# Optimization experiments

Hardware: AMD Instinct MI355X
Metric: run time of the kernel (lower is better)

Reference implementation:

```python
import jax, jax.numpy as jnp
import numpy as np

NUM_USERS = 100000
NUM_ITEMS = 50000
EMBED_DIM = 64
N_LAYERS = 3
NNZ = 4800000
BATCH = 16384
N_NODES = NUM_USERS + NUM_ITEMS


def setup_inputs() -> dict:
    key = jax.random.key(0)
    k1, k2, k3, k4, k5, k6, k7 = jax.random.split(key, 7)
    users = jax.random.randint(k1, (BATCH,), 0, NUM_USERS, dtype=jnp.int64 if jax.config.jax_enable_x64 else jnp.int32)
    items = jax.random.randint(k2, (BATCH,), 0, NUM_ITEMS, dtype=jnp.int64 if jax.config.jax_enable_x64 else jnp.int32)
    adj_rows = jax.random.randint(k3, (NNZ,), 0, N_NODES, dtype=jnp.int32)
    adj_cols = jax.random.randint(k4, (NNZ,), 0, N_NODES, dtype=jnp.int32)
    adj_vals = jax.random.uniform(k5, (NNZ,), dtype=jnp.float32)
    user_emb = jax.random.normal(k6, (NUM_USERS, EMBED_DIM), dtype=jnp.float32)
    item_emb = jax.random.normal(k7, (NUM_ITEMS, EMBED_DIM), dtype=jnp.float32)
    return {"users": users, "items": items, "adj_rows": adj_rows,
            "adj_cols": adj_cols, "adj_vals": adj_vals,
            "user_emb": user_emb, "item_emb": item_emb}


def _spmm(rows, cols, vals, x):
    # y = A @ x for COO sparse A: gather source rows, scale, scatter-add to dest
    return jax.ops.segment_sum(vals[:, None] * x[cols], rows, num_segments=N_NODES)


def reference(users, items, adj_rows, adj_cols, adj_vals, user_emb, item_emb):
    ego = jnp.concatenate([user_emb, item_emb], axis=0)  # [N_NODES, D]
    acc = ego
    cur = ego
    for _ in range(N_LAYERS):
        cur = _spmm(adj_rows, adj_cols, adj_vals, cur)
        acc = acc + cur
    mean_emb = acc / jnp.float32(N_LAYERS + 1)
    user_final = mean_emb[:NUM_USERS]
    item_final = mean_emb[NUM_USERS:]
    u = user_final[users]  # [B, D]
    i = item_final[items]  # [B, D]
    return jnp.sum(u * i, axis=-1)  # [B]
```

## Files before the change

### kernel.cpp

```cpp
#include <hip/hip_runtime.h>
#include <hip/hip_bf16.h>

#define NUM_USERS 100000
#define NUM_ITEMS 50000
#define EMBED_DIM 64
#define N_NODES   150000
#define ROW_SHIFT 9
#define ROWS_PER_BUCKET 512
#define B_BUCKETS ((N_NODES + ROWS_PER_BUCKET - 1) / ROWS_PER_BUCKET)
#define NBP 512
#define BIN_CHUNK 2048
#define PLACE_CHUNK 2048
#define COL_MASK 0x3FFFF

typedef unsigned short ushort_t;
typedef unsigned int uint_t;

__device__ __forceinline__ float bf16_to_f32(ushort_t u) {
    return __uint_as_float(((unsigned)u) << 16);
}
__device__ __forceinline__ ushort_t f32_to_bf16(float f) {
    return __builtin_bit_cast(ushort_t, __float2bfloat16(f));
}

__device__ __forceinline__ void scan512(int c, int t, int* wsum,
                                        int* excl_out, int* total_out) {
    int lane = t & 63, wv = t >> 6;
    int x = c;
#pragma unroll
    for (int d = 1; d < 64; d <<= 1) {
        int y = __shfl_up(x, d, 64);
        if (lane >= d) x += y;
    }
    if (lane == 63) wsum[wv] = x;
    __syncthreads();
    if (t < 64) {
        int s = (lane < 8) ? wsum[lane] : 0;
#pragma unroll
        for (int d = 1; d < 8; d <<= 1) {
            int y = __shfl_up(s, d, 64);
            if (lane >= d) s += y;
        }
        if (lane < 8) wsum[lane] = s;
    }
    __syncthreads();
    int off = (wv > 0) ? wsum[wv - 1] : 0;
    *excl_out = x + off - c;
    *total_out = wsum[7];
}

__global__ void __launch_bounds__(512) k_bin2(const float* __restrict__ ue,
                                              const float* __restrict__ ie,
                                              ushort_t* __restrict__ xb,
                                              const int* __restrict__ rows,
                                              const int* __restrict__ cols,
                                              const float* __restrict__ vals,
                                              int* __restrict__ cursor,
                                              int2* __restrict__ staging,
                                              int nnz, int cap, int g_conv) {
    int t = threadIdx.x;
    if ((int)blockIdx.x < g_conv) {
        int i = blockIdx.x * 512 + t;
        const int n4 = (N_NODES * EMBED_DIM) / 4;
        if (i >= n4) return;
        const int usplit = (NUM_USERS * EMBED_DIM) / 4;
        float4 f = (i < usplit) ? ((const float4*)ue)[i] : ((const float4*)ie)[i - usplit];
        ushort4 o;
        o.x = f32_to_bf16(f.x);
        o.y = f32_to_bf16(f.y);
        o.z = f32_to_bf16(f.z);
        o.w = f32_to_bf16(f.w);
        ((ushort4*)xb)[i] = o;
        return;
    }

    __shared__ int  ccnt[NBP];
    __shared__ int  cpos[NBP];
    __shared__ int  gdst[NBP];
    __shared__ int  wsum[8];
    __shared__ int2 entries[BIN_CHUNK];
    __shared__ ushort_t ebuck[BIN_CHUNK];

    int base = (blockIdx.x - g_conv) * BIN_CHUNK;
    ccnt[t] = 0;
    __syncthreads();

    int   myrow[BIN_CHUNK / 512];
    int   mycol[BIN_CHUNK / 512];
    float myval[BIN_CHUNK / 512];
#pragma unroll
    for (int k = 0; k < BIN_CHUNK / 512; k++) {
        int idx = base + k * 512 + t;
        int r = (idx < nnz) ? rows[idx] : -1;
        myrow[k] = r;
        if (r >= 0) {
            mycol[k] = cols[idx];
            myval[k] = vals[idx];
            atomicAdd(&ccnt[r >> ROW_SHIFT], 1);
        }
    }
    __syncthreads();

    int c = ccnt[t];
    int excl, total;
    scan512(c, t, wsum, &excl, &total);
    cpos[t] = excl;
    __syncthreads();

#pragma unroll
    for (int k = 0; k < BIN_CHUNK / 512; k++) {
        int r = myrow[k];
        if (r >= 0) {
            int b = r >> ROW_SHIFT;
            int lrow = r & (ROWS_PER_BUCKET - 1);
            int slot = atomicAdd(&cpos[b], 1);
            entries[slot] = make_int2(mycol[k] | (lrow << 18), __float_as_int(myval[k]));
            ebuck[slot] = (ushort_t)b;
        }
    }
    __syncthreads();

    if (t < B_BUCKETS && ccnt[t] > 0) {
        int g = atomicAdd(&cursor[t], ccnt[t]);
        gdst[t] = t * cap + g - (cpos[t] - ccnt[t]);
    }
    __syncthreads();

    for (int i = t; i < total; i += 512) {
        int eb = ebuck[i];
        int pos = gdst[eb] + i;
        if (pos < (eb + 1) * cap)
            staging[pos] = entries[i];
    }
}

__global__ void __launch_bounds__(512) k_hist(const int2* __restrict__ staging,
                                              const int* __restrict__ cursor,
                                              int* __restrict__ H,
                                              int cap, int chunks) {
    __shared__ int h[ROWS_PER_BUCKET];
    int b = blockIdx.x / chunks;
    int k = blockIdx.x - b * chunks;
    int t = threadIdx.x;
    h[t] = 0;
    __syncthreads();
    int cnt_b = cursor[b];
    if (cnt_b > cap) cnt_b = cap;
    int hi = k * PLACE_CHUNK + PLACE_CHUNK;
    if (hi > cnt_b) hi = cnt_b;
    int rbase = b * cap;
#pragma unroll 1
    for (int i = k * PLACE_CHUNK + t; i < hi; i += 512)
        atomicAdd(&h[staging[rbase + i].x >> 18], 1);
    __syncthreads();
    H[(size_t)blockIdx.x * ROWS_PER_BUCKET + t] = h[t];
}

__global__ void __launch_bounds__(512) k_scan2(int* __restrict__ H,
                                               int2* __restrict__ ranges,
                                               int cap, int chunks) {
    __shared__ int wsum[8];
    int b = blockIdx.x;
    int t = threadIdx.x;
    size_t base = (size_t)b * chunks * ROWS_PER_BUCKET + t;
    int c = 0;
#pragma unroll 1
    for (int k = 0; k < chunks; k++) c += H[base + (size_t)k * ROWS_PER_BUCKET];
    int excl, total;
    scan512(c, t, wsum, &excl, &total);
    (void)total;
    int row = (b << ROW_SHIFT) + t;
    int beg = b * cap + excl;
    if (row < N_NODES) ranges[row] = make_int2(beg, beg + c);
    int s = beg;
#pragma unroll 1
    for (int k = 0; k < chunks; k++) {
        int hh = H[base + (size_t)k * ROWS_PER_BUCKET];
        H[base + (size_t)k * ROWS_PER_BUCKET] = s;
        s += hh;
    }
}

__global__ void __launch_bounds__(512) k_place2(const int2* __restrict__ staging,
                                                const int* __restrict__ cursor,
                                                const int* __restrict__ H,
                                                int2* __restrict__ cv,
                                                int cap, int chunks) {
    __shared__ int c[ROWS_PER_BUCKET];
    int b = blockIdx.x / chunks;
    int k = blockIdx.x - b * chunks;
    int t = threadIdx.x;
    c[t] = H[(size_t)blockIdx.x * ROWS_PER_BUCKET + t];
    __syncthreads();
    int cnt_b = cursor[b];
    if (cnt_b > cap) cnt_b = cap;
    int hi = k * PLACE_CHUNK + PLACE_CHUNK;
    if (hi > cnt_b) hi = cnt_b;
    int rbase = b * cap;
#pragma unroll 1
    for (int i = k * PLACE_CHUNK + t; i < hi; i += 512) {
        int2 e = staging[rbase + i];
        int pos = atomicAdd(&c[e.x >> 18], 1);
        cv[pos] = make_int2(e.x & COL_MASK, e.y);
    }
}

#define ISSUE8(R, J0)                                                         \
    _Pragma("unroll")                                                         \
    for (int j = 0; j < 8; j++) {                                             \
        int sc = __builtin_amdgcn_readlane(vc, (J0) + j);                     \
        R[j] = xb[((size_t)(uint_t)sc << 6) + lane];                          \
    }

#define CONS8(R, J0)                                                          \
    _Pragma("unroll")                                                         \
    for (int j = 0; j < 8; j++) {                                             \
        float sv = __uint_as_float((uint_t)__builtin_amdgcn_readlane(vv, (J0) + j)); \
        acc += sv * __uint_as_float((uint_t)R[j] << 16);                      \
    }

__device__ __forceinline__ float spmm_row_rl(int beg, int end, int lane,
                                             const int2* __restrict__ cv,
                                             const ushort_t* __restrict__ xb) {
    float acc = 0.f;
#pragma unroll 1
    for (int b = beg; b < end; b += 64) {
        int2 ed = cv[b + lane];
        bool lv = (b + lane) < end;
        int vc = lv ? ed.x : 0;
        int vv = lv ? ed.y : 0;
        int rem = end - b;
        if (rem > 64) rem = 64;

        ushort_t q0[8], q1[8], q2[8], q3[8];
        ISSUE8(q0, 0)
        if (rem > 8)  { ISSUE8(q1, 8)  }
        if (rem > 16) { ISSUE8(q2, 16) }
        if (rem > 24) { ISSUE8(q3, 24) }
        CONS8(q0, 0)
        if (rem > 8)  { CONS8(q1, 8)  }
        if (rem > 16) { CONS8(q2, 16) }
        if (rem > 24) { CONS8(q3, 24) }
        if (rem > 32) {
            ISSUE8(q0, 32)
            if (rem > 40) { ISSUE8(q1, 40) }
            if (rem > 48) { ISSUE8(q2, 48) }
            if (rem > 56) { ISSUE8(q3, 56) }
            CONS8(q0, 32)
            if (rem > 40) { CONS8(q1, 40) }
            if (rem > 48) { CONS8(q2, 48) }
            if (rem > 56) { CONS8(q3, 56) }
        }
    }
    return acc;
}

__global__ void k_spmm(const int2* __restrict__ ranges, const int2* __restrict__ cv,
                       const ushort_t* __restrict__ xb, ushort_t* __restrict__ out) {
    int row = (blockIdx.x * blockDim.x + threadIdx.x) >> 6;
    int lane = threadIdx.x & 63;
    if (row >= N_NODES) return;
    row = __builtin_amdgcn_readfirstlane(row);
    int2 rng = ranges[row];
    int beg = __builtin_amdgcn_readfirstlane(rng.x);
    int end = __builtin_amdgcn_readfirstlane(rng.y);
    float a = spmm_row_rl(beg, end, lane, cv, xb);
    out[(size_t)row * 64 + lane] = f32_to_bf16(a);
}

__global__ void k_last(const int2* __restrict__ ranges, const int2* __restrict__ cv,
                       const int* __restrict__ users, const int* __restrict__ items,
                       const float* __restrict__ ue, const float* __restrict__ ie,
                       const ushort_t* __restrict__ xbA, const ushort_t* __restrict__ xbB,
                       float* __restrict__ out, int batch) {
    __shared__ float uv[2][64];
    int lane  = threadIdx.x & 63;
    int lwave = threadIdx.x >> 6;
    int gwave = (int)blockIdx.x * 4 + lwave;
    int w     = gwave >> 1;
    int side  = gwave & 1;
    bool valid = w < batch;

    int beg = 0, end = 0, row = 0, idxv = 0;
    if (valid) {
        idxv = __builtin_amdgcn_readfirstlane(side ? items[w] : users[w]);
        row  = side ? NUM_USERS + idxv : idxv;
        int2 rng = ranges[row];
        beg = __builtin_amdgcn_readfirstlane(rng.x);
        end = __builtin_amdgcn_readfirstlane(rng.y);
    }
    float a = spmm_row_rl(beg, end, lane, cv, xbB);

    float x_ = 0.f;
    if (valid) {
        float e = side ? ie[(size_t)idxv * EMBED_DIM + lane]
                       : ue[(size_t)idxv * EMBED_DIM + lane];
        float A = bf16_to_f32(xbA[(size_t)row * 64 + lane]);
        float B = bf16_to_f32(xbB[(size_t)row * 64 + lane]);
        x_ = e + A + B + a;
    }
    int slot = lwave >> 1;
    if (valid && side == 0) uv[slot][lane] = x_;
    __syncthreads();
    if (valid && side == 1) {
        float p = x_ * uv[slot][lane];
#pragma unroll
        for (int d = 32; d > 0; d >>= 1) p += __shfl_down(p, d, 64);
        if (lane == 0) out[w] = p * (1.0f / 16.0f);
    }
}


extern "C" void kernel_launch(void* const* d_in, const int* in_sizes, int n_in,
                              void* d_out, int out_size, void* d_ws, size_t ws_size,
                              hipStream_t stream) {
    const int*   users    = (const int*)  d_in[0];
    const int*   items    = (const int*)  d_in[1];
    const int*   adj_rows = (const int*)  d_in[2];
    const int*   adj_cols = (const int*)  d_in[3];
    const float* adj_vals = (const float*)d_in[4];
    const float* user_emb = (const float*)d_in[5];
    const float* item_emb = (const float*)d_in[6];
    float* out = (float*)d_out;

    const int batch = in_sizes[0];
    const int nnz   = in_sizes[2];

    int cap = ((nnz / B_BUCKETS) * 9 + 7) / 8;
    cap = (cap + 63) & ~63;
    const size_t padded = (size_t)B_BUCKETS * cap;
    const int chunks = (cap + PLACE_CHUNK - 1) / PLACE_CHUNK;

    char* p = (char*)d_ws;
    auto alloc = [&](size_t bytes) -> char* {
        char* r = p;
        p += (bytes + 255) & ~(size_t)255;
        return r;
    };
    const size_t xb_bytes = (size_t)N_NODES * EMBED_DIM * 2;
    int2*     ranges = (int2*) alloc((size_t)N_NODES * 8);
    int*      cursor = (int*)  alloc(NBP * 4);
    int*      H      = (int*)  alloc((size_t)B_BUCKETS * chunks * ROWS_PER_BUCKET * 4);
    int2*     cv     = (int2*) alloc(padded * 8);
    size_t    region_bytes = padded * 8;
    if (region_bytes < 2 * xb_bytes) region_bytes = 2 * xb_bytes;
    char*     region  = alloc(region_bytes);
    int2*     staging = (int2*)region;
    ushort_t* xbA     = (ushort_t*)region;
    ushort_t* xbB     = (ushort_t*)(region + xb_bytes);
    ushort_t* xb_ego  = (ushort_t*)alloc(xb_bytes);

    const int g_conv  = ((N_NODES * EMBED_DIM / 4) + 511) / 512;
    const int g_bin   = (nnz + BIN_CHUNK - 1) / BIN_CHUNK;
    const int g_nodes = (N_NODES + 3) / 4;
    const int g_last  = (2 * batch + 3) / 4;

    hipMemsetAsync(cursor, 0, NBP * 4, stream);
    k_bin2<<<g_conv + g_bin, 512, 0, stream>>>(user_emb, item_emb, xb_ego,
                                               adj_rows, adj_cols, adj_vals,
                                               cursor, staging, nnz, cap, g_conv);
    k_hist<<<B_BUCKETS * chunks, 512, 0, stream>>>(staging, cursor, H, cap, chunks);
    k_scan2<<<B_BUCKETS, 512, 0, stream>>>(H, ranges, cap, chunks);
    k_place2<<<B_BUCKETS * chunks, 512, 0, stream>>>(staging, cursor, H, cv,
                                                     cap, chunks);

    k_spmm<<<g_nodes, 256, 0, stream>>>(ranges, cv, xb_ego, xbA);

    k_spmm<<<g_nodes, 256, 0, stream>>>(ranges, cv, xbA, xbB);

    k_last<<<g_last, 256, 0, stream>>>(ranges, cv, users, items,
                                       user_emb, item_emb, xbA, xbB, out, batch);
}
```

Measured before the change: 422.5 us.

## Split CSR col/val arrays and load edge weights via scalar loads

Splits the interleaved column/value edge array into separate column and value arrays. Columns are still loaded per lane and broadcast with readlane, while the 64 edge weights of a chunk are fetched with inline-asm s_load_dwordx16 into scalar registers, which removes the per-edge readlane of the value. The inner accumulation is split into two accumulators to shorten the FMA dependency chain, and k_last is made branch-free for invalid waves. The cost is higher SGPR pressure, an explicit lgkmcnt wait, and scalar loads that may read past the end of a row's segment, whose results are masked out.

```diff
diff --git a/kernel.cpp b/kernel.cpp
--- a/kernel.cpp
+++ b/kernel.cpp
@@ -15,6 +15,7 @@
 
 typedef unsigned short ushort_t;
 typedef unsigned int uint_t;
+typedef __attribute__((ext_vector_type(16))) int i16;
 
 __device__ __forceinline__ float bf16_to_f32(ushort_t u) {
     return __uint_as_float(((unsigned)u) << 16);
@@ -184,7 +185,8 @@
 __global__ void __launch_bounds__(512) k_place2(const int2* __restrict__ staging,
                                                 const int* __restrict__ cursor,
                                                 const int* __restrict__ H,
-                                                int2* __restrict__ cv,
+                                                int* __restrict__ cvc,
+                                                float* __restrict__ cvv,
                                                 int cap, int chunks) {
     __shared__ int c[ROWS_PER_BUCKET];
     int b = blockIdx.x / chunks;
@@ -201,61 +203,97 @@
     for (int i = k * PLACE_CHUNK + t; i < hi; i += 512) {
         int2 e = staging[rbase + i];
         int pos = atomicAdd(&c[e.x >> 18], 1);
-        cv[pos] = make_int2(e.x & COL_MASK, e.y);
-    }
-}
+        cvc[pos] = e.x & COL_MASK;
+        cvv[pos] = __int_as_float(e.y);
+    }
+}
+
+#define SLOADV(V0, V1, V2, V3, P)                                             \
+    {                                                                         \
+        unsigned long long _a = (unsigned long long)(P);                      \
+        uint_t _lo = __builtin_amdgcn_readfirstlane((uint_t)_a);              \
+        uint_t _hi = __builtin_amdgcn_readfirstlane((uint_t)(_a >> 32));      \
+        unsigned long long _sa = (((unsigned long long)_hi) << 32) | _lo;     \
+        asm volatile("s_load_dwordx16 %0, %4, 0x0\n\t"                        \
+                     "s_load_dwordx16 %1, %4, 0x40\n\t"                       \
+                     "s_load_dwordx16 %2, %4, 0x80\n\t"                       \
+                     "s_load_dwordx16 %3, %4, 0xC0"                           \
+                     : "=&s"(V0), "=&s"(V1), "=&s"(V2), "=&s"(V3)             \
+                     : "s"(_sa));                                             \
+    }
+
+#define SFENCE(V0, V1, V2, V3)                                                \
+    asm volatile("s_waitcnt lgkmcnt(0)"                                       \
+                 : "+s"(V0), "+s"(V1), "+s"(V2), "+s"(V3) :: "memory");       \
+    __builtin_amdgcn_sched_barrier(0);
 
 #define ISSUE8(R, J0)                                                         \
     _Pragma("unroll")                                                         \
     for (int j = 0; j < 8; j++) {                                             \
-        int sc = __builtin_amdgcn_readlane(vc, (J0) + j);                     \
+        int sc = __builtin_amdgcn_readlane(vcl, (J0) + j);                    \
         R[j] = xb[((size_t)(uint_t)sc << 6) + lane];                          \
     }
 
-#define CONS8(R, J0)                                                          \
+#define CONS8U(R, VV, H)                                                      \
     _Pragma("unroll")                                                         \
-    for (int j = 0; j < 8; j++) {                                             \
-        float sv = __uint_as_float((uint_t)__builtin_amdgcn_readlane(vv, (J0) + j)); \
-        acc += sv * __uint_as_float((uint_t)R[j] << 16);                      \
-    }
+    for (int j = 0; j < 8; j += 2) {                                          \
+        acc0 += __int_as_float(VV[(H) + j])     * __uint_as_float((uint_t)R[j] << 16);     \
+        acc1 += __int_as_float(VV[(H) + j + 1]) * __uint_as_float((uint_t)R[j + 1] << 16); \
+    }
+
+#define CONS8G(R, VV, H, J0)                                                  \
+    _Pragma("unroll")                                                         \
+    for (int j = 0; j < 8; j += 2) {                                          \
+        float s0 = ((J0) + j     < rem) ? __int_as_float(VV[(H) + j])     : 0.f; \
+        float s1 = ((J0) + j + 1 < rem) ? __int_as_float(VV[(H) + j + 1]) : 0.f; \
+        acc0 += s0 * __uint_as_float((uint_t)R[j] << 16);                     \
+        acc1 += s1 * __uint_as_float((uint_t)R[j + 1] << 16);                 \
+    }
+
+#define CGROUP(R, VV, H, J0)                                                  \
+    if (rem >= (J0) + 8) { CONS8U(R, VV, H) } else { CONS8G(R, VV, H, J0) }
 
 __device__ __forceinline__ float spmm_row_rl(int beg, int end, int lane,
-                                             const int2* __restrict__ cv,
+                                             const int* __restrict__ cvc,
+                                             const float* __restrict__ cvv,
                                              const ushort_t* __restrict__ xb) {
-    float acc = 0.f;
+    float acc0 = 0.f, acc1 = 0.f;
 #pragma unroll 1
     for (int b = beg; b < end; b += 64) {
-        int2 ed = cv[b + lane];
-        bool lv = (b + lane) < end;
-        int vc = lv ? ed.x : 0;
-        int vv = lv ? ed.y : 0;
+        int vc = cvc[b + lane];
+        int vcl = (b + lane) < end ? vc : 0;
         int rem = end - b;
         if (rem > 64) rem = 64;
+
+        i16 V0, V1, V2, V3;
+        SLOADV(V0, V1, V2, V3, cvv + b)
 
         ushort_t q0[8], q1[8], q2[8], q3[8];
         ISSUE8(q0, 0)
         if (rem > 8)  { ISSUE8(q1, 8)  }
         if (rem > 16) { ISSUE8(q2, 16) }
         if (rem > 24) { ISSUE8(q3, 24) }
-        CONS8(q0, 0)
-        if (rem > 8)  { CONS8(q1, 8)  }
-        if (rem > 16) { CONS8(q2, 16) }
-        if (rem > 24) { CONS8(q3, 24) }
+        SFENCE(V0, V1, V2, V3)
+        CGROUP(q0, V0, 0, 0)
+        if (rem > 8)  { CGROUP(q1, V0, 8, 8)  }
+        if (rem > 16) { CGROUP(q2, V1, 0, 16) }
+        if (rem > 24) { CGROUP(q3, V1, 8, 24) }
         if (rem > 32) {
             ISSUE8(q0, 32)
             if (rem > 40) { ISSUE8(q1, 40) }
             if (rem > 48) { ISSUE8(q2, 48) }
             if (rem > 56) { ISSUE8(q3, 56) }
-            CONS8(q0, 32)
-            if (rem > 40) { CONS8(q1, 40) }
-            if (rem > 48) { CONS8(q2, 48) }
-            if (rem > 56) { CONS8(q3, 56) }
+            CGROUP(q0, V2, 0, 32)
+            if (rem > 40) { CGROUP(q1, V2, 8, 40) }
+            if (rem > 48) { CGROUP(q2, V3, 0, 48) }
+            if (rem > 56) { CGROUP(q3, V3, 8, 56) }
         }
     }
-    return acc;
-}
-
-__global__ void k_spmm(const int2* __restrict__ ranges, const int2* __restrict__ cv,
+    return acc0 + acc1;
+}
+
+__global__ void k_spmm(const int2* __restrict__ ranges, const int* __restrict__ cvc,
+                       const float* __restrict__ cvv,
                        const ushort_t* __restrict__ xb, ushort_t* __restrict__ out) {
     int row = (blockIdx.x * blockDim.x + threadIdx.x) >> 6;
     int lane = threadIdx.x & 63;
@@ -264,11 +302,12 @@
     int2 rng = ranges[row];
     int beg = __builtin_amdgcn_readfirstlane(rng.x);
     int end = __builtin_amdgcn_readfirstlane(rng.y);
-    float a = spmm_row_rl(beg, end, lane, cv, xb);
+    float a = spmm_row_rl(beg, end, lane, cvc, cvv, xb);
     out[(size_t)row * 64 + lane] = f32_to_bf16(a);
 }
 
-__global__ void k_last(const int2* __restrict__ ranges, const int2* __restrict__ cv,
+__global__ void k_last(const int2* __restrict__ ranges, const int* __restrict__ cvc,
+                       const float* __restrict__ cvv,
                        const int* __restrict__ users, const int* __restrict__ items,
                        const float* __restrict__ ue, const float* __restrict__ ie,
                        const ushort_t* __restrict__ xbA, const ushort_t* __restrict__ xbB,
@@ -280,25 +319,21 @@
     int w     = gwave >> 1;
     int side  = gwave & 1;
     bool valid = w < batch;
-
-    int beg = 0, end = 0, row = 0, idxv = 0;
-    if (valid) {
-        idxv = __builtin_amdgcn_readfirstlane(side ? items[w] : users[w]);
-        row  = side ? NUM_USERS + idxv : idxv;
-        int2 rng = ranges[row];
-        beg = __builtin_amdgcn_readfirstlane(rng.x);
-        end = __builtin_amdgcn_readfirstlane(rng.y);
-    }
-    float a = spmm_row_rl(beg, end, lane, cv, xbB);
-
-    float x_ = 0.f;
-    if (valid) {
-        float e = side ? ie[(size_t)idxv * EMBED_DIM + lane]
-                       : ue[(size_t)idxv * EMBED_DIM + lane];
-        float A = bf16_to_f32(xbA[(size_t)row * 64 + lane]);
-        float B = bf16_to_f32(xbB[(size_t)row * 64 + lane]);
-        x_ = e + A + B + a;
-    }
+    int wc    = valid ? w : batch - 1;
+
+    int idxv = __builtin_amdgcn_readfirstlane(side ? items[wc] : users[wc]);
+    int row  = side ? NUM_USERS + idxv : idxv;
+    int2 rng = ranges[row];
+    int beg  = __builtin_amdgcn_readfirstlane(rng.x);
+    int end  = __builtin_amdgcn_readfirstlane(valid ? rng.y : rng.x);
+    float a = spmm_row_rl(beg, end, lane, cvc, cvv, xbB);
+
+    float e = side ? ie[(size_t)idxv * EMBED_DIM + lane]
+                   : ue[(size_t)idxv * EMBED_DIM + lane];
+    float A = bf16_to_f32(xbA[(size_t)row * 64 + lane]);
+    float B = bf16_to_f32(xbB[(size_t)row * 64 + lane]);
+    float x_ = e + A + B + a;
+
     int slot = lwave >> 1;
     if (valid && side == 0) uv[slot][lane] = x_;
     __syncthreads();
@@ -341,7 +376,8 @@
     int2*     ranges = (int2*) alloc((size_t)N_NODES * 8);
     int*      cursor = (int*)  alloc(NBP * 4);
     int*      H      = (int*)  alloc((size_t)B_BUCKETS * chunks * ROWS_PER_BUCKET * 4);
-    int2*     cv     = (int2*) alloc(padded * 8);
+    int*      cvc    = (int*)  alloc(padded * 4);
+    float*    cvv    = (float*)alloc(padded * 4);
     size_t    region_bytes = padded * 8;
     if (region_bytes < 2 * xb_bytes) region_bytes = 2 * xb_bytes;
     char*     region  = alloc(region_bytes);
@@ -361,13 +397,13 @@
                                                cursor, staging, nnz, cap, g_conv);
     k_hist<<<B_BUCKETS * chunks, 512, 0, stream>>>(staging, cursor, H, cap, chunks);
     k_scan2<<<B_BUCKETS, 512, 0, stream>>>(H, ranges, cap, chunks);
-    k_place2<<<B_BUCKETS * chunks, 512, 0, stream>>>(staging, cursor, H, cv,
-                                                     cap, chunks);
-
-    k_spmm<<<g_nodes, 256, 0, stream>>>(ranges, cv, xb_ego, xbA);
-
-    k_spmm<<<g_nodes, 256, 0, stream>>>(ranges, cv, xbA, xbB);
-
-    k_last<<<g_last, 256, 0, stream>>>(ranges, cv, users, items,
+    k_place2<<<B_BUCKETS * chunks, 512, 0, stream>>>(staging, cursor, H,
+                                                     cvc, cvv, cap, chunks);
+
+    k_spmm<<<g_nodes, 256, 0, stream>>>(ranges, cvc, cvv, xb_ego, xbA);
+
+    k_spmm<<<g_nodes, 256, 0, stream>>>(ranges, cvc, cvv, xbA, xbB);
+
+    k_last<<<g_last, 256, 0, stream>>>(ranges, cvc, cvv, users, items,
                                        user_emb, item_emb, xbA, xbB, out, batch);
 }
```

After: 502.6 us. 19.0% more time.
